# Kernel optimization log

Measured on AMD Instinct MI355X. Metric: run time of the kernel, lower is better.

Reference implementation:

```python
import jax, jax.numpy as jnp
import numpy as np

K = 100          # n_neighbours
JITTER = 1e-6    # numerical stabilizer for the normal-equations solve


def setup_inputs() -> dict:
    key = jax.random.key(0)
    k1, k2, k3, k4 = jax.random.split(key, 4)
    B, D, N = 1024, 64, 100000
    return {
        "input": jax.random.normal(k1, (B, D), dtype=jnp.float32),
        "target": jax.random.normal(k2, (B, 1), dtype=jnp.float32),
        "db_X": jax.random.normal(k3, (N, D), dtype=jnp.float32),
        "db_y": jax.random.normal(k4, (N, 1), dtype=jnp.float32),
    }


def reference(input, target, db_X, db_y):
    B, D = input.shape
    # Per-row MSE distance to every db point: mean over feature dim.
    # ||x - d||^2 / D  expanded to avoid materializing [B, N, D].
    x2 = jnp.sum(input * input, axis=1, keepdims=True)           # [B, 1]
    d2 = jnp.sum(db_X * db_X, axis=1)                            # [N]
    dist = (x2 - 2.0 * (input @ db_X.T) + d2) / D                # [B, N]

    # k smallest distances -> neighbor indices
    _, idx = jax.lax.top_k(-dist, K)                             # [B, K]

    Xn = db_X[idx]                                               # [B, K, D]
    yn = db_y[idx]                                               # [B, K, 1]

    ones_k = jnp.ones((B, K, 1), dtype=input.dtype)
    A = jnp.concatenate([ones_k, Xn], axis=-1)                   # [B, K, D+1]
    AtA = jnp.einsum('bkp,bkq->bpq', A, A)                       # [B, D+1, D+1]
    Aty = jnp.einsum('bkp,bko->bpo', A, yn)                      # [B, D+1, 1]
    eye = jnp.eye(D + 1, dtype=input.dtype)
    beta = jnp.linalg.solve(AtA + JITTER * eye, Aty)             # [B, D+1, 1]

    # Predict at the query row itself
    xa = jnp.concatenate([jnp.ones((B, 1), dtype=input.dtype), input], axis=-1)  # [B, D+1]
    preds = jnp.einsum('bp,bpo->bo', xa, beta)                   # [B, 1]

    # MSELoss with reduction='mean'
    return jnp.mean(jnp.square(preds - target))
```

## Files before the change

### kernel.cpp

```cpp
#include <hip/hip_runtime.h>

#define N_DB   100000
#define B_Q    1024
#define D_F    64
#define K_NN   100
#define JITTER 1e-6f
#define NS     12544
#define STGT   40
#define NT     782
#define SLOT   16
#define CAP    3072
#define BB     512
#define TP     80
#define AST    68

typedef __attribute__((ext_vector_type(8))) short bf16x8;
typedef __attribute__((ext_vector_type(4))) float f32x4;

__device__ __forceinline__ unsigned short f2b(float x) {
    unsigned u = __float_as_uint(x);
    u += 0x7FFF + ((u >> 16) & 1);
    return (unsigned short)(u >> 16);
}

__global__ __launch_bounds__(256) void k_prep(
    const float* __restrict__ db_X, const float* __restrict__ input,
    unsigned short* __restrict__ dbb, unsigned short* __restrict__ inb,
    float* __restrict__ d2, float* __restrict__ x2) {
    int tid = threadIdx.x;
    int lane = tid & 63;
    int sub = lane & 15, grp = lane >> 4;
    int row = blockIdx.x * 16 + (tid >> 6) * 4 + grp;
    const int R = N_DB + B_Q;
    if (row >= R) return;
    const float* src = (row < N_DB) ? db_X + (size_t)row * 64 + sub * 4
                                    : input + (size_t)(row - N_DB) * 64 + sub * 4;
    unsigned short* dst = (row < N_DB) ? dbb + (size_t)row * 64 + sub * 4
                                       : inb + (size_t)(row - N_DB) * 64 + sub * 4;
    float4 w = *(const float4*)src;
    ushort4 o = { f2b(w.x), f2b(w.y), f2b(w.z), f2b(w.w) };
    *(ushort4*)dst = o;
    float s = w.x * w.x + w.y * w.y + w.z * w.z + w.w * w.w;
    s += __shfl_xor(s, 1, 64);
    s += __shfl_xor(s, 2, 64);
    s += __shfl_xor(s, 4, 64);
    s += __shfl_xor(s, 8, 64);
    if (sub == 0) {
        if (row < N_DB) d2[row] = s;
        else            x2[row - N_DB] = s;
    }
}

__device__ __forceinline__ void stage_rows_bf16(
    const unsigned short* __restrict__ src, unsigned short* dst,
    int n0, int tid, bool guard) {
    #pragma unroll
    for (int it = 0; it < 4; it++) {
        int f = it * 256 + tid;
        int c = f >> 3, k8 = f & 7;
        int n = n0 + c;
        uint4 w = make_uint4(0u, 0u, 0u, 0u);
        if (!guard || n < N_DB) w = *(const uint4*)(src + (size_t)n * 64 + k8 * 8);
        *(uint4*)(&dst[c * TP + k8 * 8]) = w;
    }
}

__device__ __forceinline__ void mfma_tile(
    const unsigned short* As, const unsigned short* Bs,
    int wr, int wc, int fr, int fq, f32x4 acc[4][4]) {
    #pragma unroll
    for (int ks = 0; ks < 2; ks++) {
        int koff = fq * 8 + ks * 32;
        bf16x8 a[4], b[4];
        #pragma unroll
        for (int i = 0; i < 4; i++)
            a[i] = *(const bf16x8*)(&As[(wr + i * 16 + fr) * TP + koff]);
        #pragma unroll
        for (int j = 0; j < 4; j++)
            b[j] = *(const bf16x8*)(&Bs[(wc + j * 16 + fr) * TP + koff]);
        #pragma unroll
        for (int i = 0; i < 4; i++)
            #pragma unroll
            for (int j = 0; j < 4; j++)
                acc[i][j] = __builtin_amdgcn_mfma_f32_16x16x32_bf16(a[i], b[j], acc[i][j], 0, 0, 0);
    }
}

__global__ __launch_bounds__(256) void k_gemm_sample(
    const unsigned short* __restrict__ inb, const unsigned short* __restrict__ dbb,
    const float* __restrict__ x2, const float* __restrict__ d2,
    unsigned char* __restrict__ sbin) {
    __shared__ unsigned short As[128 * TP];
    __shared__ unsigned short Bs[128 * TP];
    __shared__ float x2s[128], d2s[128];
    int tid = threadIdx.x;
    int n0 = blockIdx.x * 128;
    int b0 = blockIdx.y * 128;

    stage_rows_bf16(dbb, Bs, n0, tid, false);
    stage_rows_bf16(inb, As, b0, tid, false);
    if (tid < 128) {
        d2s[tid] = d2[n0 + tid];
        x2s[tid] = x2[b0 + tid];
    }
    __syncthreads();

    int lane = tid & 63, wid = tid >> 6;
    int wr = (wid >> 1) * 64, wc = (wid & 1) * 64;
    int fr = lane & 15, fq = lane >> 4;
    f32x4 acc[4][4];
    #pragma unroll
    for (int i = 0; i < 4; i++)
        #pragma unroll
        for (int j = 0; j < 4; j++) acc[i][j] = (f32x4){0.f, 0.f, 0.f, 0.f};
    mfma_tile(As, Bs, wr, wc, fr, fq, acc);

    const float inv_d = 1.0f / D_F;
    int jsel = fr >> 2;
    int base_src = (fq << 4) | (4 * (fr & 3));
    #pragma unroll
    for (int i = 0; i < 4; i++) {
        #pragma unroll
        for (int r = 0; r < 4; r++) {
            int row = wr + i * 16 + fq * 4 + r;
            float xx = x2s[row];
            unsigned p = 0;
            #pragma unroll
            for (int j = 0; j < 4; j++) {
                int col = wc + j * 16 + fr;
                float dv = (xx + d2s[col] - 2.0f * acc[i][j][r]) * inv_d;
                int bin = (int)(dv * 64.0f);
                bin = bin < 0 ? 0 : (bin > 255 ? 255 : bin);
                p |= (unsigned)bin << (8 * j);
            }
            unsigned out = 0;
            #pragma unroll
            for (int e = 0; e < 4; e++) {
                unsigned q = __shfl(p, base_src + e, 64);
                out |= ((q >> (8 * jsel)) & 255u) << (8 * e);
            }
            int ncol = n0 + wc + 4 * fr;
            *(unsigned*)(sbin + (size_t)(b0 + row) * NS + ncol) = out;
        }
    }
}

__global__ __launch_bounds__(256) void k_thr(
    const unsigned char* __restrict__ sbin, int* __restrict__ thr_t) {
    int b = blockIdx.x, tid = threadIdx.x;
    __shared__ int hist[256];
    hist[tid] = 0;
    __syncthreads();
    const uint4* row4 = (const uint4*)(sbin + (size_t)b * NS);
    for (int v = tid; v < NS / 16; v += 256) {
        uint4 w = row4[v];
        unsigned ws[4] = {w.x, w.y, w.z, w.w};
        #pragma unroll
        for (int q = 0; q < 4; q++)
            #pragma unroll
            for (int e = 0; e < 4; e++)
                atomicAdd(&hist[(ws[q] >> (8 * e)) & 255u], 1);
    }
    __syncthreads();
    if (tid == 0) {
        int cum = 0, t = 255;
        for (int i = 0; i < 256; i++) {
            cum += hist[i];
            if (cum >= STGT) { t = i; break; }
        }
        thr_t[b] = t;
    }
}

__global__ __launch_bounds__(256) void k_gemm_cand(
    const unsigned short* __restrict__ inb, const unsigned short* __restrict__ dbb,
    const float* __restrict__ x2, const float* __restrict__ d2,
    const int* __restrict__ thr_t, unsigned char* __restrict__ counts,
    unsigned char* __restrict__ nle2, unsigned* __restrict__ cand2) {
    __shared__ unsigned short As[128 * TP];
    __shared__ unsigned short Bs[128 * TP];
    __shared__ float d2h[128], rl[128], rt[128];
    __shared__ int rowcnt[128], rtc[128];
    __shared__ unsigned slots[128 * SLOT];
    int tid = threadIdx.x;
    int n0 = blockIdx.x * 128;
    int b0 = blockIdx.y * 128;

    stage_rows_bf16(dbb, Bs, n0, tid, true);
    stage_rows_bf16(inb, As, b0, tid, false);
    if (tid < 128) {
        int n = n0 + tid;
        d2h[tid] = (n < N_DB) ? d2[n] * 0.5f : 1e30f;
        float xx = x2[b0 + tid];
        int t = thr_t[b0 + tid];
        rl[tid] = (xx - (float)(t + 3)) * 0.5f;
        rt[tid] = (xx - (float)(t + 1)) * 0.5f;
        rowcnt[tid] = 0; rtc[tid] = 0;
    }
    __syncthreads();

    int lane = tid & 63, wid = tid >> 6;
    int wr = (wid >> 1) * 64, wc = (wid & 1) * 64;
    int fr = lane & 15, fq = lane >> 4;
    f32x4 acc[4][4];
    #pragma unroll
    for (int i = 0; i < 4; i++)
        #pragma unroll
        for (int j = 0; j < 4; j++) acc[i][j] = (f32x4){0.f, 0.f, 0.f, 0.f};
    mfma_tile(As, Bs, wr, wc, fr, fq, acc);

    #pragma unroll
    for (int i = 0; i < 4; i++) {
        #pragma unroll
        for (int r = 0; r < 4; r++) {
            int row = wr + i * 16 + fq * 4 + r;
            float rlv = rl[row], rtv = rt[row];
            #pragma unroll
            for (int j = 0; j < 4; j++) {
                int col = wc + j * 16 + fr;
                float a = acc[i][j][r];
                float dh = d2h[col];
                if (a > rlv + dh) {
                    int pos = atomicAdd(&rowcnt[row], 1);
                    if (pos < SLOT) slots[row * SLOT + pos] = (unsigned)(n0 + col);
                    if (a > rtv + dh) atomicAdd(&rtc[row], 1);
                }
            }
        }
    }
    __syncthreads();

    size_t gb = (size_t)blockIdx.x * B_Q + b0;
    if (tid < 128) {
        int rc = rowcnt[tid]; counts[gb + tid] = (unsigned char)(rc > 255 ? 255 : rc);
        int tc = rtc[tid];    nle2[gb + tid]   = (unsigned char)(tc > 255 ? 255 : tc);
    }
    for (int e = tid; e < 128 * SLOT; e += 256)
        cand2[gb * SLOT + e] = slots[e];
}

__global__ __launch_bounds__(256) void k_refine(
    const unsigned char* __restrict__ counts, const unsigned char* __restrict__ nle2,
    const unsigned* __restrict__ cand2, const float* __restrict__ input,
    const float* __restrict__ db_X, const float* __restrict__ x2,
    const float* __restrict__ d2, float* __restrict__ cdG, int* __restrict__ ciG,
    int* __restrict__ cntF, int* __restrict__ nleF, int* __restrict__ badF) {
    int b = blockIdx.x, tid = threadIdx.x, lane = tid & 63;
    __shared__ float xrow[64];
    __shared__ int lidx[CAP];
    __shared__ int s_cnt, s_nle, s_bad;
    if (tid < 64) xrow[tid] = input[(size_t)b * 64 + tid];
    if (tid == 0) { s_cnt = 0; s_nle = 0; s_bad = 0; }
    __syncthreads();

    int tight = 0, bad = 0;
    for (int t = tid; t < NT; t += 256) {
        int c = counts[(size_t)t * B_Q + b];
        tight += nle2[(size_t)t * B_Q + b];
        if (c > SLOT) { bad = 1; c = SLOT; }
        const unsigned* sp = cand2 + ((size_t)t * B_Q + b) * SLOT;
        for (int e = 0; e < c; e++) {
            int pos = atomicAdd(&s_cnt, 1);
            if (pos < CAP) lidx[pos] = (int)sp[e];
            else bad = 1;
        }
    }
    #pragma unroll
    for (int off = 32; off; off >>= 1) tight += __shfl_xor(tight, off, 64);
    if (lane == 0) atomicAdd(&s_nle, tight);
    if (bad) atomicOr(&s_bad, 1);
    __syncthreads();

    int cn = s_cnt > CAP ? CAP : s_cnt;
    float xx = x2[b];
    for (int c = tid; c < cn; c += 256) {
        int n = lidx[c];
        const float4* dr = (const float4*)(db_X + (size_t)n * D_F);
        float dot = 0.f;
        #pragma unroll
        for (int k = 0; k < 16; k++) {
            float4 w = dr[k];
            dot += xrow[k * 4 + 0] * w.x + xrow[k * 4 + 1] * w.y
                 + xrow[k * 4 + 2] * w.z + xrow[k * 4 + 3] * w.w;
        }
        cdG[(size_t)b * CAP + c] = (xx - 2.0f * dot + d2[n]) * (1.0f / D_F);
        ciG[(size_t)b * CAP + c] = n;
    }
    if (tid == 0) {
        cntF[b] = cn;
        nleF[b] = s_nle;
        badF[b] = s_bad;
    }
}

__global__ __launch_bounds__(256) void k_rank(
    const int* __restrict__ cntF, const int* __restrict__ nleF,
    const int* __restrict__ badF, const float* __restrict__ cdG,
    const int* __restrict__ ciG, const int* __restrict__ thr_t,
    const float* __restrict__ input, const float* __restrict__ db_X,
    const float* __restrict__ x2, const float* __restrict__ d2,
    int* __restrict__ idx) {
    int b = blockIdx.x, tid = threadIdx.x;
    __shared__ float ldist[CAP];
    __shared__ int lidx[CAP];
    __shared__ int hist[1024];
    __shared__ int s4[256];
    __shared__ float bbd[BB];
    __shared__ int bbn[BB];
    __shared__ int s_b100, s_c0, s_out, s_bb;
    __shared__ float xrow[64];

    if (tid < 64) xrow[tid] = input[(size_t)b * 64 + tid];
    #pragma unroll
    for (int h = 0; h < 4; h++) hist[h * 256 + tid] = 0;
    if (tid == 0) { s_out = 0; s_bb = 0; }
    __syncthreads();

    int cn = cntF[b];
    bool bad = (badF[b] != 0) || (nleF[b] < K_NN);
    float xx = x2[b];

    float sc;
    if (!bad) {
        float hi = (float)(thr_t[b] + 4) * (1.0f / 64.0f);
        sc = 1024.0f / hi;
        for (int c = tid; c < cn; c += 256) {
            float d = cdG[(size_t)b * CAP + c];
            ldist[c] = d;
            lidx[c] = ciG[(size_t)b * CAP + c];
            int bn = (int)(d * sc);
            bn = bn < 0 ? 0 : (bn > 1023 ? 1023 : bn);
            atomicAdd(&hist[bn], 1);
        }
    } else {
        sc = 256.0f;
        for (int n = tid; n < N_DB; n += 256) {
            const float4* dr = (const float4*)(db_X + (size_t)n * D_F);
            float dot = 0.f;
            #pragma unroll
            for (int k = 0; k < 16; k++) {
                float4 w = dr[k];
                dot += xrow[k * 4 + 0] * w.x + xrow[k * 4 + 1] * w.y
                     + xrow[k * 4 + 2] * w.z + xrow[k * 4 + 3] * w.w;
            }
            float d = (xx - 2.0f * dot + d2[n]) * (1.0f / D_F);
            int bn = (int)(d * sc);
            bn = bn < 0 ? 0 : (bn > 1023 ? 1023 : bn);
            atomicAdd(&hist[bn], 1);
        }
    }
    __syncthreads();

    {
        int t4 = hist[4 * tid] + hist[4 * tid + 1] + hist[4 * tid + 2] + hist[4 * tid + 3];
        s4[tid] = t4;
    }
    __syncthreads();
    if (tid == 0) {
        int cum = 0, bsel = 1023, c0 = 0;
        for (int g = 0; g < 256; g++) {
            if (cum + s4[g] >= K_NN) {
                int c2 = cum;
                bsel = g * 4 + 3;
                for (int e = 0; e < 4; e++) {
                    if (c2 + hist[g * 4 + e] >= K_NN) { bsel = g * 4 + e; break; }
                    c2 += hist[g * 4 + e];
                }
                c0 = c2;
                break;
            }
            cum += s4[g];
        }
        s_b100 = bsel; s_c0 = c0;
    }
    __syncthreads();
    int b100 = s_b100, c0 = s_c0;

    if (!bad) {
        for (int c = tid; c < cn; c += 256) {
            float d = ldist[c];
            int bn = (int)(d * sc);
            bn = bn < 0 ? 0 : (bn > 1023 ? 1023 : bn);
            if (bn < b100) {
                int pos = atomicAdd(&s_out, 1);
                idx[(size_t)b * K_NN + pos] = lidx[c];
            } else if (bn == b100) {
                int pos = atomicAdd(&s_bb, 1);
                if (pos < BB) { bbd[pos] = d; bbn[pos] = lidx[c]; }
            }
        }
    } else {
        for (int n = tid; n < N_DB; n += 256) {
            const float4* dr = (const float4*)(db_X + (size_t)n * D_F);
            float dot = 0.f;
            #pragma unroll
            for (int k = 0; k < 16; k++) {
                float4 w = dr[k];
                dot += xrow[k * 4 + 0] * w.x + xrow[k * 4 + 1] * w.y
                     + xrow[k * 4 + 2] * w.z + xrow[k * 4 + 3] * w.w;
            }
            float d = (xx - 2.0f * dot + d2[n]) * (1.0f / D_F);
            int bn = (int)(d * sc);
            bn = bn < 0 ? 0 : (bn > 1023 ? 1023 : bn);
            if (bn < b100) {
                int pos = atomicAdd(&s_out, 1);
                idx[(size_t)b * K_NN + pos] = n;
            } else if (bn == b100) {
                int pos = atomicAdd(&s_bb, 1);
                if (pos < BB) { bbd[pos] = d; bbn[pos] = n; }
            }
        }
    }
    __syncthreads();

    int m = K_NN - c0;
    int bc = s_bb; if (bc > BB) bc = BB;
    for (int c = tid; c < bc; c += 256) {
        float dc = bbd[c]; int nc = bbn[c];
        int rank = 0;
        for (int j = 0; j < bc; j++) {
            float dj = bbd[j];
            rank += (dj < dc) || (dj == dc && bbn[j] < nc);
        }
        if (rank < m) {
            int pos = atomicAdd(&s_out, 1);
            idx[(size_t)b * K_NN + pos] = nc;
        }
    }
}

__global__ __launch_bounds__(256) void k_regress(
    const float* __restrict__ input, const float* __restrict__ target,
    const float* __restrict__ db_X, const float* __restrict__ db_y,
    const int* __restrict__ idx, float* __restrict__ out) {
    int b = blockIdx.x, tid = threadIdx.x;
    __shared__ float A[K_NN * AST];
    __shared__ float M[65 * AST];
    __shared__ float v[65], xa[68], yv[K_NN];
    __shared__ int nbr[K_NN];

    if (tid < K_NN) {
        int n = idx[(size_t)b * K_NN + tid];
        nbr[tid] = n;
        yv[tid] = db_y[n];
    }
    if (tid < 64) xa[1 + tid] = input[(size_t)b * D_F + tid];
    if (tid == 0) { xa[0] = 1.f; xa[65] = xa[66] = xa[67] = 0.f; }
    __syncthreads();

    for (int f = tid; f < K_NN * AST; f += 256) {
        int k = f / AST, c = f - k * AST;
        float val = 0.f;
        if (c == 0) val = 1.f;
        else if (c <= 64) val = db_X[(size_t)nbr[k] * D_F + (c - 1)];
        A[f] = val;
    }
    __syncthreads();

    for (int tsk = tid; tsk < 289; tsk += 256) {
        int ti = tsk / 17, tj = tsk % 17;
        int p0 = ti * 4, q0 = tj * 4;
        float acc[4][4];
        #pragma unroll
        for (int ii = 0; ii < 4; ii++)
            #pragma unroll
            for (int jj = 0; jj < 4; jj++) acc[ii][jj] = 0.f;
        for (int k = 0; k < K_NN; k++) {
            float4 ap = *(const float4*)(&A[k * AST + p0]);
            float4 aq = *(const float4*)(&A[k * AST + q0]);
            float app[4] = {ap.x, ap.y, ap.z, ap.w};
            float aqq[4] = {aq.x, aq.y, aq.z, aq.w};
            #pragma unroll
            for (int ii = 0; ii < 4; ii++)
                #pragma unroll
                for (int jj = 0; jj < 4; jj++) acc[ii][jj] += app[ii] * aqq[jj];
        }
        #pragma unroll
        for (int ii = 0; ii < 4; ii++)
            #pragma unroll
            for (int jj = 0; jj < 4; jj++) {
                int p = p0 + ii, q = q0 + jj;
                if (p < 65 && q < 65)
                    M[p * AST + q] = acc[ii][jj] + (p == q ? JITTER : 0.f);
            }
    }
    for (int p = tid; p < 65; p += 256) {
        float s = 0.f;
        for (int k = 0; k < K_NN; k++) s += A[k * AST + p] * yv[k];
        M[p * AST + 65] = s;
    }
    __syncthreads();

    for (int j = 0; j < 65; j++) {
        float inv = 1.0f / M[j * AST + j];
        for (int c = j + 1 + (tid & 63); c <= 65; c += 64) {
            float mjc = M[j * AST + c] * inv;
            for (int i = j + 1 + (tid >> 6); i <= 64; i += 4)
                M[i * AST + c] -= M[i * AST + j] * mjc;
        }
        __syncthreads();
    }

    if (tid < 64) {
        int i = tid;
        float ri = M[i * AST + 65];
        float di = M[i * AST + i];
        float x64 = M[64 * AST + 65] / M[64 * AST + 64];
        ri -= M[i * AST + 64] * x64;
        float xi_out = 0.f;
        for (int j = 63; j >= 0; j--) {
            float xj = __shfl(ri, j, 64) / __shfl(di, j, 64);
            if (i == j) xi_out = xj;
            if (i < j) ri -= M[i * AST + j] * xj;
        }
        v[i] = xi_out;
        if (i == 0) v[64] = x64;
    }
    __syncthreads();

    if (tid == 0) {
        float pred = 0.f;
        for (int q = 0; q <= 64; q++) pred += xa[q] * v[q];
        float e = pred - target[b];
        atomicAdd(out, e * e * (1.0f / B_Q));
    }
}

extern "C" void kernel_launch(void* const* d_in, const int* in_sizes, int n_in,
                              void* d_out, int out_size, void* d_ws, size_t ws_size,
                              hipStream_t stream) {
    const float* input  = (const float*)d_in[0];
    const float* target = (const float*)d_in[1];
    const float* db_X   = (const float*)d_in[2];
    const float* db_y   = (const float*)d_in[3];
    float* out = (float*)d_out;

    char* ws = (char*)d_ws;
    size_t off = 0;
    auto alloc = [&](size_t bytes) {
        size_t o = off;
        off += (bytes + 255) & ~(size_t)255;
        return o;
    };
    float*    d2    = (float*)(ws + alloc((size_t)N_DB * 4));
    float*    x2    = (float*)(ws + alloc((size_t)B_Q * 4));
    int*      idx   = (int*)(ws + alloc((size_t)B_Q * K_NN * 4));
    int*      thr_t = (int*)(ws + alloc((size_t)B_Q * 4));
    int*      cntF  = (int*)(ws + alloc((size_t)B_Q * 4));
    int*      nleF  = (int*)(ws + alloc((size_t)B_Q * 4));
    int*      badF  = (int*)(ws + alloc((size_t)B_Q * 4));
    unsigned char* counts = (unsigned char*)(ws + alloc((size_t)NT * B_Q));
    unsigned char* nle2   = (unsigned char*)(ws + alloc((size_t)NT * B_Q));
    unsigned* cand2 = (unsigned*)(ws + alloc((size_t)NT * B_Q * SLOT * 4));
    float*    cdG   = (float*)(ws + alloc((size_t)B_Q * CAP * 4));
    int*      ciG   = (int*)(ws + alloc((size_t)B_Q * CAP * 4));
    unsigned short* dbb = (unsigned short*)(ws + alloc((size_t)N_DB * 64 * 2));
    unsigned short* inb = (unsigned short*)(ws + alloc((size_t)B_Q * 64 * 2));
    unsigned char*  sbin = (unsigned char*)(ws + alloc((size_t)B_Q * NS));

    hipMemsetAsync(d_out, 0, sizeof(float) * out_size, stream);

    k_prep<<<(N_DB + B_Q + 15) / 16, 256, 0, stream>>>(db_X, input, dbb, inb, d2, x2);
    {
        dim3 g(NS / 128, B_Q / 128);
        k_gemm_sample<<<g, 256, 0, stream>>>(inb, dbb, x2, d2, sbin);
    }
    k_thr<<<B_Q, 256, 0, stream>>>(sbin, thr_t);
    {
        dim3 g(NT, B_Q / 128);
        k_gemm_cand<<<g, 256, 0, stream>>>(inb, dbb, x2, d2, thr_t, counts, nle2, cand2);
    }
    k_refine<<<B_Q, 256, 0, stream>>>(counts, nle2, cand2, input, db_X, x2, d2,
                                      cdG, ciG, cntF, nleF, badF);
    k_rank<<<B_Q, 256, 0, stream>>>(cntF, nleF, badF, cdG, ciG, thr_t,
                                    input, db_X, x2, d2, idx);
    k_regress<<<B_Q, 256, 0, stream>>>(input, target, db_X, db_y, idx, out);
}
```

Baseline: 355.5 us.

## Block the Gaussian elimination in four columns and exploit AtA symmetry

The per-query regression kernel now gathers neighbour rows with float4 loads, computes only the upper-triangular 4x4 tiles of AtA and mirrors them, and runs Aty on a separate wavefront at the same time. The 65-step elimination, which needed a barrier per column, becomes 17 blocked steps: one wavefront factors a 4-column panel and then all waves apply a rank-4 update. The final dot product becomes a wave shuffle reduction. This reduces barrier count and redundant FLOPs, but serialises panel work on a single wave and may change rounding order.

After: 393.1 us. 1.11x slower.

```diff
diff --git a/kernel.cpp b/kernel.cpp
--- a/kernel.cpp
+++ b/kernel.cpp
@@ -434,10 +434,13 @@
     const float* __restrict__ db_X, const float* __restrict__ db_y,
     const int* __restrict__ idx, float* __restrict__ out) {
     int b = blockIdx.x, tid = threadIdx.x;
+    int lane = tid & 63, wid = tid >> 6;
     __shared__ float A[K_NN * AST];
     __shared__ float M[65 * AST];
-    __shared__ float v[65], xa[68], yv[K_NN];
+    __shared__ float v[65], xa[68];
+    __shared__ float yv[K_NN];
     __shared__ int nbr[K_NN];
+    __shared__ float s_inv[4];
 
     if (tid < K_NN) {
         int n = idx[(size_t)b * K_NN + tid];
@@ -448,17 +451,24 @@
     if (tid == 0) { xa[0] = 1.f; xa[65] = xa[66] = xa[67] = 0.f; }
     __syncthreads();
 
-    for (int f = tid; f < K_NN * AST; f += 256) {
-        int k = f / AST, c = f - k * AST;
-        float val = 0.f;
-        if (c == 0) val = 1.f;
-        else if (c <= 64) val = db_X[(size_t)nbr[k] * D_F + (c - 1)];
-        A[f] = val;
-    }
-    __syncthreads();
-
-    for (int tsk = tid; tsk < 289; tsk += 256) {
-        int ti = tsk / 17, tj = tsk % 17;
+    for (int f = tid; f < K_NN * 16; f += 256) {
+        int k = f >> 4, q = f & 15;
+        float4 w = *(const float4*)(db_X + (size_t)nbr[k] * D_F + q * 4);
+        A[k * AST + 1 + q * 4 + 0] = w.x;
+        A[k * AST + 1 + q * 4 + 1] = w.y;
+        A[k * AST + 1 + q * 4 + 2] = w.z;
+        A[k * AST + 1 + q * 4 + 3] = w.w;
+    }
+    if (tid < K_NN) {
+        A[tid * AST + 0] = 1.0f;
+        A[tid * AST + 65] = 0.f; A[tid * AST + 66] = 0.f; A[tid * AST + 67] = 0.f;
+    }
+    __syncthreads();
+
+    if (tid < 153) {
+        int ti = 0, rem = tid;
+        while (rem >= 17 - ti) { rem -= 17 - ti; ti++; }
+        int tj = ti + rem;
         int p0 = ti * 4, q0 = tj * 4;
         float acc[4][4];
         #pragma unroll
@@ -480,23 +490,66 @@
             #pragma unroll
             for (int jj = 0; jj < 4; jj++) {
                 int p = p0 + ii, q = q0 + jj;
-                if (p < 65 && q < 65)
-                    M[p * AST + q] = acc[ii][jj] + (p == q ? JITTER : 0.f);
-            }
-    }
-    for (int p = tid; p < 65; p += 256) {
+                if (p < 65 && q < 65) {
+                    float val = acc[ii][jj] + (p == q ? JITTER : 0.f);
+                    M[p * AST + q] = val;
+                    if (ti != tj) M[q * AST + p] = val;
+                }
+            }
+    } else if (tid >= 192) {
+        int p = tid - 192;
         float s = 0.f;
         for (int k = 0; k < K_NN; k++) s += A[k * AST + p] * yv[k];
         M[p * AST + 65] = s;
-    }
-    __syncthreads();
-
-    for (int j = 0; j < 65; j++) {
-        float inv = 1.0f / M[j * AST + j];
-        for (int c = j + 1 + (tid & 63); c <= 65; c += 64) {
-            float mjc = M[j * AST + c] * inv;
-            for (int i = j + 1 + (tid >> 6); i <= 64; i += 4)
-                M[i * AST + c] -= M[i * AST + j] * mjc;
+        if (tid == 192) {
+            float s2 = 0.f;
+            for (int k = 0; k < K_NN; k++) s2 += A[k * AST + 64] * yv[k];
+            M[64 * AST + 65] = s2;
+        }
+    }
+    __syncthreads();
+
+    for (int jb = 0; jb < 17; jb++) {
+        int j0 = jb * 4;
+        int jend = (j0 + 4 < 65) ? j0 + 4 : 65;
+        int np = jend - j0;
+        if (wid == 0) {
+            #pragma unroll
+            for (int l4 = 0; l4 < 4; l4++) {
+                int l = j0 + l4;
+                if (l4 < np) {
+                    float inv = 1.0f / M[l * AST + l];
+                    if (lane == 0) s_inv[l4] = inv;
+                    for (int i = l + 1; i < jend; i++) {
+                        float mil = M[i * AST + l] * inv;
+                        for (int c = l + 1 + lane; c < 66; c += 64)
+                            M[i * AST + c] -= mil * M[l * AST + c];
+                    }
+                }
+            }
+        }
+        __syncthreads();
+        float inv0 = s_inv[0], inv1 = s_inv[1], inv2 = s_inv[2], inv3 = s_inv[3];
+        for (int i = jend + (tid >> 6); i < 65; i += 4) {
+            float a0 = M[i * AST + j0] * inv0;
+            float a1 = 0.f, a2 = 0.f, a3 = 0.f;
+            if (np > 1)
+                a1 = (M[i * AST + j0 + 1] - a0 * M[j0 * AST + j0 + 1]) * inv1;
+            if (np > 2)
+                a2 = (M[i * AST + j0 + 2] - a0 * M[j0 * AST + j0 + 2]
+                                          - a1 * M[(j0 + 1) * AST + j0 + 2]) * inv2;
+            if (np > 3)
+                a3 = (M[i * AST + j0 + 3] - a0 * M[j0 * AST + j0 + 3]
+                                          - a1 * M[(j0 + 1) * AST + j0 + 3]
+                                          - a2 * M[(j0 + 2) * AST + j0 + 3]) * inv3;
+            for (int c = jend + lane; c < 66; c += 64) {
+                float m = M[i * AST + c];
+                m -= a0 * M[j0 * AST + c];
+                if (np > 1) m -= a1 * M[(j0 + 1) * AST + c];
+                if (np > 2) m -= a2 * M[(j0 + 2) * AST + c];
+                if (np > 3) m -= a3 * M[(j0 + 3) * AST + c];
+                M[i * AST + c] = m;
+            }
         }
         __syncthreads();
     }
@@ -518,11 +571,15 @@
     }
     __syncthreads();
 
-    if (tid == 0) {
-        float pred = 0.f;
-        for (int q = 0; q <= 64; q++) pred += xa[q] * v[q];
-        float e = pred - target[b];
-        atomicAdd(out, e * e * (1.0f / B_Q));
+    if (wid == 0) {
+        float p = xa[lane] * v[lane];
+        if (lane == 0) p += xa[64] * v[64];
+        #pragma unroll
+        for (int off = 32; off; off >>= 1) p += __shfl_xor(p, off, 64);
+        if (lane == 0) {
+            float e = p - target[b];
+            atomicAdd(out, e * e * (1.0f / B_Q));
+        }
     }
 }
 
```
